# Kernel tuning notes

Measured on AMD Instinct MI355X. Metric: run time of the kernel, lower is better.

The kernel has to match this reference:

```python
import jax, jax.numpy as jnp
from jax import lax
import numpy as np

SEQ_LEN, INPUT_DIM, HID, NCLS, BATCH = 1024, 1, 512, 10, 256


def setup_inputs() -> dict:
    key = jax.random.key(0)
    k1, k2, k3, k4 = jax.random.split(key, 4)
    def xavier(k, shape):
        fan_in, fan_out = shape[1], shape[0]
        bound = np.sqrt(6.0 / (fan_in + fan_out))
        return jax.random.uniform(k, shape, jnp.float32, -bound, bound)
    return {
        "x": jax.random.normal(k1, (BATCH, SEQ_LEN), jnp.float32),
        "h_init": jnp.zeros((HID, 1), jnp.float32),
        "W_hx": xavier(k2, (HID, INPUT_DIM)),
        "W_hh": xavier(k3, (HID, HID)),
        "b_h": jnp.zeros((HID, 1), jnp.float32),
        "W_ph": xavier(k4, (NCLS, HID)),
        "b_p": jnp.zeros((NCLS, 1), jnp.float32),
    }


def reference(x, h_init, W_hx, W_hh, b_h, W_ph, b_p):
    # x: [B, T] scalar inputs per step (input_dim == 1)
    B = x.shape[0]
    H = h_init.shape[0]
    # Broadcasting h_init [H,1] to [H,B] up-front is mathematically identical
    # to the torch code (W_hh @ h_init broadcasts against [H,B] at step 0).
    h0 = jnp.broadcast_to(h_init, (H, B))

    def step(h, x_t):
        # x_t: [B]; W_hx @ x_t[None,:] -> [H, B]
        h_new = jnp.tanh(W_hx @ x_t[None, :] + W_hh @ h + b_h)
        return h_new, None

    h_last, _ = lax.scan(step, h0, x.T)  # scan over time axis [T, B]
    p = W_ph @ h_last + b_p  # [NCLS, B]
    return p.T  # [B, NCLS]
```

## Files before the change

kernel.cpp:

```cpp
#include <hip/hip_runtime.h>


#define T_SEQ    1024
#define HID      512
#define NTHREADS 512
#define NW       8
#define NCLS     10
#define RP       8
#define PAIRS    32
#define PREG     28
#define PLDS     4

typedef _Float16 half2_t __attribute__((ext_vector_type(2)));

__device__ __forceinline__ unsigned int pack2(float a, float b) {
    half2_t h = {(_Float16)a, (_Float16)b};
    return __builtin_bit_cast(unsigned int, h);
}

__device__ __forceinline__ float dot2(unsigned int w, unsigned int h, float acc) {
#if __has_builtin(__builtin_amdgcn_fdot2)
    return __builtin_amdgcn_fdot2(__builtin_bit_cast(half2_t, w),
                                  __builtin_bit_cast(half2_t, h), acc, false);
#else
    half2_t wv = __builtin_bit_cast(half2_t, w), hv = __builtin_bit_cast(half2_t, h);
    return acc + (float)wv.x * (float)hv.x + (float)wv.y * (float)hv.y;
#endif
}

__global__ __attribute__((amdgpu_flat_work_group_size(NTHREADS, NTHREADS)))
           __attribute__((amdgpu_waves_per_eu(2, 2)))
void rnn_persist(
    const float* __restrict__ x, const float* __restrict__ h_init,
    const float* __restrict__ W_hx, const float* __restrict__ W_hh,
    const float* __restrict__ b_h, const float* __restrict__ W_ph,
    const float* __restrict__ b_p, float* __restrict__ out)
{
    __shared__ uint4  Wl[NW * RP * 64];
    __shared__ float  part[2][NW][HID];
    __shared__ float  x_s[T_SEQ];
    __shared__ _Float16 hs[HID];

    const int tid  = threadIdx.x;
    const int b    = blockIdx.x;
    const int w    = tid >> 6;
    const int lane = tid & 63;

    for (int i = tid; i < T_SEQ; i += NTHREADS) x_s[i] = x[(size_t)b * T_SEQ + i];

    const float whx = W_hx[tid];
    const float bh  = b_h[tid];
    hs[tid] = (_Float16)h_init[tid];

    unsigned int wreg[RP][PREG];
    #pragma unroll
    for (int r = 0; r < RP; ++r) {
        const float4* row = (const float4*)(W_hh + (size_t)(RP * lane + r) * HID + 64 * w);
        unsigned int p32[PAIRS];
        #pragma unroll
        for (int q = 0; q < 16; ++q) {
            float4 v = row[q];
            p32[2 * q]     = pack2(v.x, v.y);
            p32[2 * q + 1] = pack2(v.z, v.w);
        }
        #pragma unroll
        for (int p = 0; p < PREG; ++p) wreg[r][p] = p32[p];
        Wl[(w * RP + r) * 64 + lane] = make_uint4(p32[28], p32[29], p32[30], p32[31]);
    }
    __syncthreads();

    const unsigned int* hsw = (const unsigned int*)hs + w * (PAIRS);

    float hval = 0.0f;
    for (int t = 0; t < T_SEQ; ++t) {
        const int buf = t & 1;

        float acc[RP];
        #pragma unroll
        for (int r = 0; r < RP; ++r) acc[r] = 0.0f;

        #pragma unroll
        for (int p = 0; p < PREG; ++p) {
            unsigned int hp = hsw[p];
            #pragma unroll
            for (int r = 0; r < RP; ++r) acc[r] = dot2(wreg[r][p], hp, acc[r]);
        }
        {
            unsigned int h0 = hsw[28], h1 = hsw[29], h2 = hsw[30], h3 = hsw[31];
            #pragma unroll
            for (int r = 0; r < RP; ++r) {
                uint4 wq = Wl[(w * RP + r) * 64 + lane];
                acc[r] = dot2(wq.x, h0, acc[r]);
                acc[r] = dot2(wq.y, h1, acc[r]);
                acc[r] = dot2(wq.z, h2, acc[r]);
                acc[r] = dot2(wq.w, h3, acc[r]);
            }
        }

        float4* pw = (float4*)&part[buf][w][RP * lane];
        pw[0] = make_float4(acc[0], acc[1], acc[2], acc[3]);
        pw[1] = make_float4(acc[4], acc[5], acc[6], acc[7]);

        __syncthreads();

        float s = whx * x_s[t] + bh;
        #pragma unroll
        for (int j = 0; j < NW; ++j) s += part[buf][j][tid];

        hval = 1.0f - 2.0f / (__expf(2.0f * s) + 1.0f);
        hs[tid] = (_Float16)hval;
    }

    __syncthreads();
    x_s[tid] = hval;
    __syncthreads();

    for (int c = w; c < NCLS; c += NW) {
        float s = 0.0f;
        #pragma unroll
        for (int j = 0; j < 8; ++j) {
            int r = lane + 64 * j;
            s += W_ph[c * HID + r] * x_s[r];
        }
        #pragma unroll
        for (int off = 32; off; off >>= 1) s += __shfl_down(s, off, 64);
        if (lane == 0) out[b * NCLS + c] = s + b_p[c];
    }
}

extern "C" void kernel_launch(void* const* d_in, const int* in_sizes, int n_in,
                              void* d_out, int out_size, void* d_ws, size_t ws_size,
                              hipStream_t stream) {
    const float* x      = (const float*)d_in[0];
    const float* h_init = (const float*)d_in[1];
    const float* W_hx   = (const float*)d_in[2];
    const float* W_hh   = (const float*)d_in[3];
    const float* b_h    = (const float*)d_in[4];
    const float* W_ph   = (const float*)d_in[5];
    const float* b_p    = (const float*)d_in[6];
    float* out = (float*)d_out;

    const int B = in_sizes[0] / T_SEQ;
    rnn_persist<<<B, NTHREADS, 0, stream>>>(x, h_init, W_hx, W_hh, b_h, W_ph, b_p, out);
}
```

Baseline: 1.481 ms.

## Shift more W_hh pairs to LDS and pad partial-sum buffer against bank conflicts

Reduces the register-resident weight pairs per row from 28 to 26 and moves the extra two pairs into a new LDS array. This frees VGPRs and removes the temporary p32 staging array, with a scheduling barrier added to keep the load-time register footprint down. It also pads the partial-sum buffer by 4 floats every 32 entries so the float4 writes and the strided reduction reads spread across LDS banks. The trade-off is extra LDS reads of weights on every timestep.

```diff
diff --git a/kernel.cpp b/kernel.cpp
--- a/kernel.cpp
+++ b/kernel.cpp
@@ -8,8 +8,8 @@
 #define NCLS     10
 #define RP       8
 #define PAIRS    32
-#define PREG     28
-#define PLDS     4
+#define PREG     26
+#define PSTRIDE  576
 
 typedef _Float16 half2_t __attribute__((ext_vector_type(2)));
 
@@ -28,6 +28,8 @@
 #endif
 }
 
+__device__ __forceinline__ int pidx(int row) { return row + ((row >> 5) << 2); }
+
 __global__ __attribute__((amdgpu_flat_work_group_size(NTHREADS, NTHREADS)))
            __attribute__((amdgpu_waves_per_eu(2, 2)))
 void rnn_persist(
@@ -36,8 +38,9 @@
     const float* __restrict__ b_h, const float* __restrict__ W_ph,
     const float* __restrict__ b_p, float* __restrict__ out)
 {
-    __shared__ uint4  Wl[NW * RP * 64];
-    __shared__ float  part[2][NW][HID];
+    __shared__ uint4  Wl4[NW * RP * 64];
+    __shared__ uint2  Wl2[NW * RP * 64];
+    __shared__ float  part[2][NW][PSTRIDE];
     __shared__ float  x_s[T_SEQ];
     __shared__ _Float16 hs[HID];
 
@@ -56,20 +59,25 @@
     #pragma unroll
     for (int r = 0; r < RP; ++r) {
         const float4* row = (const float4*)(W_hh + (size_t)(RP * lane + r) * HID + 64 * w);
-        unsigned int p32[PAIRS];
         #pragma unroll
-        for (int q = 0; q < 16; ++q) {
+        for (int q = 0; q < 13; ++q) {
             float4 v = row[q];
-            p32[2 * q]     = pack2(v.x, v.y);
-            p32[2 * q + 1] = pack2(v.z, v.w);
+            wreg[r][2 * q]     = pack2(v.x, v.y);
+            wreg[r][2 * q + 1] = pack2(v.z, v.w);
         }
-        #pragma unroll
-        for (int p = 0; p < PREG; ++p) wreg[r][p] = p32[p];
-        Wl[(w * RP + r) * 64 + lane] = make_uint4(p32[28], p32[29], p32[30], p32[31]);
+        float4 v13 = row[13], v14 = row[14], v15 = row[15];
+        Wl4[(w * RP + r) * 64 + lane] =
+            make_uint4(pack2(v13.x, v13.y), pack2(v13.z, v13.w),
+                       pack2(v14.x, v14.y), pack2(v14.z, v14.w));
+        Wl2[(w * RP + r) * 64 + lane] =
+            make_uint2(pack2(v15.x, v15.y), pack2(v15.z, v15.w));
+#if __has_builtin(__builtin_amdgcn_sched_barrier)
+        __builtin_amdgcn_sched_barrier(0);
+#endif
     }
     __syncthreads();
 
-    const unsigned int* hsw = (const unsigned int*)hs + w * (PAIRS);
+    const unsigned int* hsw = (const unsigned int*)hs + w * PAIRS;
 
     float hval = 0.0f;
     for (int t = 0; t < T_SEQ; ++t) {
@@ -86,26 +94,30 @@
             for (int r = 0; r < RP; ++r) acc[r] = dot2(wreg[r][p], hp, acc[r]);
         }
         {
-            unsigned int h0 = hsw[28], h1 = hsw[29], h2 = hsw[30], h3 = hsw[31];
+            unsigned int h0 = hsw[26], h1 = hsw[27], h2 = hsw[28],
+                         h3 = hsw[29], h4 = hsw[30], h5 = hsw[31];
             #pragma unroll
             for (int r = 0; r < RP; ++r) {
-                uint4 wq = Wl[(w * RP + r) * 64 + lane];
+                uint4 wq = Wl4[(w * RP + r) * 64 + lane];
+                uint2 wd = Wl2[(w * RP + r) * 64 + lane];
                 acc[r] = dot2(wq.x, h0, acc[r]);
                 acc[r] = dot2(wq.y, h1, acc[r]);
                 acc[r] = dot2(wq.z, h2, acc[r]);
                 acc[r] = dot2(wq.w, h3, acc[r]);
+                acc[r] = dot2(wd.x, h4, acc[r]);
+                acc[r] = dot2(wd.y, h5, acc[r]);
             }
         }
 
-        float4* pw = (float4*)&part[buf][w][RP * lane];
-        pw[0] = make_float4(acc[0], acc[1], acc[2], acc[3]);
-        pw[1] = make_float4(acc[4], acc[5], acc[6], acc[7]);
+        *(float4*)&part[buf][w][pidx(RP * lane)]     = make_float4(acc[0], acc[1], acc[2], acc[3]);
+        *(float4*)&part[buf][w][pidx(RP * lane + 4)] = make_float4(acc[4], acc[5], acc[6], acc[7]);
 
         __syncthreads();
 
         float s = whx * x_s[t] + bh;
+        const int pi = pidx(tid);
         #pragma unroll
-        for (int j = 0; j < NW; ++j) s += part[buf][j][tid];
+        for (int j = 0; j < NW; ++j) s += part[buf][j][pi];
 
         hval = 1.0f - 2.0f / (__expf(2.0f * s) + 1.0f);
         hs[tid] = (_Float16)hval;
```

Result: slower. 1.762 ms (+19.0%).
